# Kernel tuning notes

Measured on AMD Instinct MI355X. Metric: run time of the kernel, lower is better.

The kernel has to match this reference:

```python
import jax, jax.numpy as jnp
import numpy as np


def setup_inputs() -> dict:
    key = jax.random.key(0)
    k1, k2 = jax.random.split(key)
    x = jax.random.normal(k1, (32, 256, 32, 32), dtype=jnp.float32)
    emb = jax.random.uniform(k2, (256, 2048), dtype=jnp.float32)
    return {"x": x, "emb": emb}


def reference(x, emb):
    # x: (B, D, H, W), emb: (D, K)
    B, D = x.shape[0], x.shape[1]
    spatial = x.shape[2:]
    K = emb.shape[1]
    # flatten latents: (N, D) with N = B*H*W
    xf = jnp.moveaxis(x, 1, -1).reshape(-1, D)
    d2 = (jnp.sum(xf * xf, axis=-1, keepdims=True)
          - 2.0 * (xf @ emb)
          + jnp.sum(emb * emb, axis=0))  # (N, K)
    argmin = jnp.argmin(d2, axis=-1)  # (N,)
    q = jnp.take(emb.T, argmin, axis=0)  # (N, D) nearest codes
    out = q.reshape(B, *spatial, D)
    out = jnp.moveaxis(out, -1, 1)  # (B, D, H, W)
    return out
```

## Files before the change

### kernel.cpp

```cpp
#include <hip/hip_runtime.h>


typedef __attribute__((ext_vector_type(8))) _Float16 half8v;
typedef __attribute__((ext_vector_type(16))) float floatx16;
typedef unsigned int uint;
typedef unsigned short ushort;

#define DD 256
#define KK 2048
#define SS 1024
#define NN 32768
#define MT 128
#define NTT 256
#define CD 32
#define LDA 40
#define MFMA_F16 __builtin_amdgcn_mfma_f32_32x32x16_f16

union HU { _Float16 f; ushort u; };

__device__ __forceinline__ void split16(float v, ushort& h, ushort& l) {
    HU a, b;
    a.f = (_Float16)v;
    b.f = (_Float16)(v - (float)a.f);
    h = a.u; l = b.u;
}

__device__ __forceinline__ uint pk(ushort a, ushort b) {
    return (uint)a | ((uint)b << 16);
}

__global__ __launch_bounds__(256) void hn_kernel(const float* __restrict__ emb,
                                                 float* __restrict__ hn) {
    __shared__ float red[256];
    const int tid = threadIdx.x;
    const int k = blockIdx.x * 32 + (tid & 31);
    const int j = tid >> 5;
    float a = 0.f;
#pragma unroll
    for (int i = 0; i < 32; ++i) {
        float e = emb[(size_t)(j * 32 + i) * KK + k];
        a += e * e;
    }
    red[tid] = a;
    __syncthreads();
    if (j == 0) {
        float s = a;
#pragma unroll
        for (int g = 1; g < 8; ++g) s += red[g * 32 + (tid & 31)];
        hn[k] = 0.5f * s;
    }
}

__global__ __launch_bounds__(256) void pack_emb(const float* __restrict__ emb,
                                                uint4* __restrict__ epk) {
    int idx = blockIdx.x * 256 + threadIdx.x;
    int k = idx & (KK - 1);
    int q = idx >> 11;
    ushort h[8], l[8];
#pragma unroll
    for (int j = 0; j < 8; ++j) {
        float e = emb[(size_t)(8 * q + j) * KK + k];
        split16(e, h[j], l[j]);
    }
    uint4 H, L;
    H.x = pk(h[0], h[1]); H.y = pk(h[2], h[3]);
    H.z = pk(h[4], h[5]); H.w = pk(h[6], h[7]);
    L.x = pk(l[0], l[1]); L.y = pk(l[2], l[3]);
    L.z = pk(l[4], l[5]); L.w = pk(l[6], l[7]);
    epk[(size_t)(q * 2 + 0) * KK + k] = H;
    epk[(size_t)(q * 2 + 1) * KK + k] = L;
}

template <bool PRE>
__global__ __launch_bounds__(1024, 4) void vq_fused(
        const float* __restrict__ x, const float* __restrict__ emb,
        const float* __restrict__ hn, const uint4* __restrict__ epk,
        float* __restrict__ out) {
    __shared__ ushort Ah[2][MT * LDA], Al[2][MT * LDA];
    __shared__ ushort Bh[2][NTT * LDA], Bl[2][NTT * LDA];
    __shared__ float sv[4][MT];
    __shared__ int   sc[4][MT];
    __shared__ int   bc[MT];

    const int tid = threadIdx.x;
    const int lane = tid & 63;
    const int wid = tid >> 6;
    const int colk = lane & 31;
    const int half = lane >> 5;
    const int wm = (wid & 3) * 32;
    const int wn = (wid >> 2) * 64;

    const int base_n = blockIdx.x * MT;
    const int bq = base_n >> 10;
    const int sb = base_n & (SS - 1);

    const int lat_a = tid & 127;
    const int d2a = tid >> 7;
    const int cod_b = tid & 255;
    const int pB = (tid >> 8) & 1;
    const int oB = tid >> 9;

    const float* xA = x + ((size_t)bq * DD + 2 * d2a) * SS + sb + lat_a;

    floatx16 acc[2];
#pragma unroll
    for (int j = 0; j < 2; ++j) acc[j] = (floatx16)(0.0f);

    float bestv[16];
    int bestc[16];
#pragma unroll
    for (int r = 0; r < 16; ++r) { bestv[r] = 3.4e38f; bestc[r] = 0; }

    float fa0[4], fa1[4];
    uint4 u00, u01, u10, u11;
    float fb0[16], fb1[16];

    auto issueA = [&](int c, float (&fa)[4]) {
        const int dt = (c & 7) * CD;
        fa[0] = xA[(size_t)(dt + 0) * SS];
        fa[1] = xA[(size_t)(dt + 1) * SS];
        fa[2] = xA[(size_t)(dt + 16) * SS];
        fa[3] = xA[(size_t)(dt + 17) * SS];
    };
    auto issueB = [&](int c, uint4& a0, uint4& a1, float (&fb)[16]) {
        const int kt = c >> 3;
        const int dt = (c & 7) * CD;
        if constexpr (PRE) {
            const int qg = (dt >> 3) + 2 * oB;
            const size_t kb = (size_t)kt * NTT + cod_b;
            a0 = epk[(size_t)(qg * 2 + pB) * KK + kb];
            a1 = epk[(size_t)((qg + 1) * 2 + pB) * KK + kb];
        } else {
#pragma unroll
            for (int i = 0; i < 16; ++i)
                fb[i] = emb[(size_t)(dt + oB * 16 + i) * KK
                            + (size_t)kt * NTT + cod_b];
        }
    };
    auto stageWrite = [&](int nxt, float (&fa)[4], uint4& a0, uint4& a1,
                          float (&fb)[16]) {
        ushort h0, l0, h1, l1, h2, l2, h3, l3;
        split16(fa[0], h0, l0); split16(fa[1], h1, l1);
        split16(fa[2], h2, l2); split16(fa[3], h3, l3);
        *reinterpret_cast<uint*>(&Ah[nxt][lat_a * LDA + 2 * d2a]) = pk(h0, h1);
        *reinterpret_cast<uint*>(&Al[nxt][lat_a * LDA + 2 * d2a]) = pk(l0, l1);
        *reinterpret_cast<uint*>(&Ah[nxt][lat_a * LDA + 2 * d2a + 16]) = pk(h2, h3);
        *reinterpret_cast<uint*>(&Al[nxt][lat_a * LDA + 2 * d2a + 16]) = pk(l2, l3);
        uint4 w0, w1;
        if constexpr (PRE) {
            w0 = a0; w1 = a1;
        } else {
            ushort hh[16], ll[16];
#pragma unroll
            for (int i = 0; i < 16; ++i) split16(fb[i], hh[i], ll[i]);
            const ushort* s = pB ? ll : hh;
            w0.x = pk(s[0], s[1]);   w0.y = pk(s[2], s[3]);
            w0.z = pk(s[4], s[5]);   w0.w = pk(s[6], s[7]);
            w1.x = pk(s[8], s[9]);   w1.y = pk(s[10], s[11]);
            w1.z = pk(s[12], s[13]); w1.w = pk(s[14], s[15]);
        }
        ushort* Bp = pB ? &Bl[nxt][0] : &Bh[nxt][0];
        *reinterpret_cast<uint4*>(&Bp[cod_b * LDA + oB * 16]) = w0;
        *reinterpret_cast<uint4*>(&Bp[cod_b * LDA + oB * 16 + 8]) = w1;
    };
    auto compute = [&](int cur) {
        const int fo = colk * LDA + half * 8;
#pragma unroll
        for (int t = 0; t < 2; ++t) {
            const int o = t * 16;
            half8v ah = *reinterpret_cast<const half8v*>(&Ah[cur][fo + wm * LDA + o]);
            half8v al = *reinterpret_cast<const half8v*>(&Al[cur][fo + wm * LDA + o]);
            half8v bh0 = *reinterpret_cast<const half8v*>(&Bh[cur][fo + wn * LDA + o]);
            half8v bh1 = *reinterpret_cast<const half8v*>(&Bh[cur][fo + (wn + 32) * LDA + o]);
            half8v bl0 = *reinterpret_cast<const half8v*>(&Bl[cur][fo + wn * LDA + o]);
            half8v bl1 = *reinterpret_cast<const half8v*>(&Bl[cur][fo + (wn + 32) * LDA + o]);

            acc[0] = MFMA_F16(ah, bh0, acc[0], 0, 0, 0);
            acc[0] = MFMA_F16(ah, bl0, acc[0], 0, 0, 0);
            acc[0] = MFMA_F16(al, bh0, acc[0], 0, 0, 0);

            acc[1] = MFMA_F16(ah, bh1, acc[1], 0, 0, 0);
            acc[1] = MFMA_F16(ah, bl1, acc[1], 0, 0, 0);
            acc[1] = MFMA_F16(al, bh1, acc[1], 0, 0, 0);
        }
    };
    auto epilogue = [&](int kt) {
        const int cd0 = kt * NTT + wn + colk;
        const int cd1 = cd0 + 32;
        const float h0 = hn[cd0];
        const float h1 = hn[cd1];
#pragma unroll
        for (int r = 0; r < 16; ++r) {
            float s0 = h0 - acc[0][r];
            float s1 = h1 - acc[1][r];
            float v = s0; int cd = cd0;
            if (s1 < s0) { v = s1; cd = cd1; }
            if (v < bestv[r]) { bestv[r] = v; bestc[r] = cd; }
            acc[0][r] = 0.f;
            acc[1][r] = 0.f;
        }
    };

    issueA(0, fa0); issueB(0, u00, u01, fb0);
    stageWrite(0, fa0, u00, u01, fb0);
    issueA(1, fa1); issueB(1, u10, u11, fb1);
    __syncthreads();

    for (int cc = 0; cc < 32; ++cc) {
        const int c0 = cc * 2;
        if (c0 + 2 < 64) { issueA(c0 + 2, fa0); issueB(c0 + 2, u00, u01, fb0); }
        stageWrite(1, fa1, u10, u11, fb1);
        compute(0);
        __syncthreads();

        const int c1 = c0 + 1;
        if (c1 + 2 < 64) { issueA(c1 + 2, fa1); issueB(c1 + 2, u10, u11, fb1); }
        if (c1 + 1 < 64) { stageWrite(0, fa0, u00, u01, fb0); }
        compute(1);
        if ((c1 & 7) == 7) epilogue(c1 >> 3);
        __syncthreads();
    }

#pragma unroll
    for (int r = 0; r < 16; ++r) {
        float v = bestv[r];
        int cd = bestc[r];
#pragma unroll
        for (int mk = 1; mk < 32; mk <<= 1) {
            float ov = __shfl_xor(v, mk);
            int oc = __shfl_xor(cd, mk);
            if (ov < v || (ov == v && oc < cd)) { v = ov; cd = oc; }
        }
        if (colk == 0) {
            const int row = (r & 3) + 8 * (r >> 2) + 4 * half;
            sv[wid >> 2][wm + row] = v;
            sc[wid >> 2][wm + row] = cd;
        }
    }
    __syncthreads();
    if (tid < MT) {
        float v = sv[0][tid]; int cd = sc[0][tid];
#pragma unroll
        for (int g = 1; g < 4; ++g) {
            float ov = sv[g][tid]; int oc = sc[g][tid];
            if (ov < v || (ov == v && oc < cd)) { v = ov; cd = oc; }
        }
        bc[tid] = cd;
    }
    __syncthreads();
    {
        const int mq = tid & 31;
        const int dg = tid >> 5;
        const int k0 = bc[mq * 4 + 0];
        const int k1 = bc[mq * 4 + 1];
        const int k2 = bc[mq * 4 + 2];
        const int k3 = bc[mq * 4 + 3];
#pragma unroll 4
        for (int dd = 0; dd < 8; ++dd) {
            const int d = dg * 8 + dd;
            const float* er = emb + (size_t)d * KK;
            float4 o = make_float4(er[k0], er[k1], er[k2], er[k3]);
            reinterpret_cast<float4*>(&out[((size_t)bq * DD + d) * SS + sb])[mq] = o;
        }
    }
}

extern "C" void kernel_launch(void* const* d_in, const int* in_sizes, int n_in,
                              void* d_out, int out_size, void* d_ws, size_t ws_size,
                              hipStream_t stream) {
    const float* x = (const float*)d_in[0];
    const float* emb = (const float*)d_in[1];
    float* out = (float*)d_out;
    float* hn = (float*)d_ws;
    uint4* epk = (uint4*)((char*)d_ws + KK * sizeof(float));

    const size_t need = (size_t)KK * 4 + (size_t)32 * 2 * KK * 16;

    hipLaunchKernelGGL(hn_kernel, dim3(KK / 32), dim3(256), 0, stream, emb, hn);
    if (ws_size >= need) {
        hipLaunchKernelGGL(pack_emb, dim3(65536 / 256), dim3(256), 0, stream,
                           emb, epk);
        hipLaunchKernelGGL((vq_fused<true>), dim3(NN / MT), dim3(1024), 0, stream,
                           x, emb, hn, epk, out);
    } else {
        hipLaunchKernelGGL((vq_fused<false>), dim3(NN / MT), dim3(1024), 0, stream,
                           x, emb, hn, epk, out);
    }
}
```

Before: 211.5 us.

## Load A fragments directly from global into registers, dropping A shared-memory staging

Removes the double-buffered shared-memory tiles for the x operand. Each lane now loads its own MFMA A-fragment values straight from global memory and splits them into fp16 hi/lo parts in registers right before the MFMAs. This cuts LDS writes and reads and frees shared memory. In exchange, the A loads are issued in the same iteration they are used, no longer prefetched two stages ahead, so global latency is exposed. The 4 wn-waves also each reload the same x values redundantly.

```diff
diff --git a/kernel.cpp b/kernel.cpp
--- a/kernel.cpp
+++ b/kernel.cpp
@@ -17,6 +17,7 @@
 #define MFMA_F16 __builtin_amdgcn_mfma_f32_32x32x16_f16
 
 union HU { _Float16 f; ushort u; };
+union FragU { uint u[4]; half8v v; };
 
 __device__ __forceinline__ void split16(float v, ushort& h, ushort& l) {
     HU a, b;
@@ -76,7 +77,6 @@
         const float* __restrict__ x, const float* __restrict__ emb,
         const float* __restrict__ hn, const uint4* __restrict__ epk,
         float* __restrict__ out) {
-    __shared__ ushort Ah[2][MT * LDA], Al[2][MT * LDA];
     __shared__ ushort Bh[2][NTT * LDA], Bl[2][NTT * LDA];
     __shared__ float sv[4][MT];
     __shared__ int   sc[4][MT];
@@ -94,13 +94,11 @@
     const int bq = base_n >> 10;
     const int sb = base_n & (SS - 1);
 
-    const int lat_a = tid & 127;
-    const int d2a = tid >> 7;
     const int cod_b = tid & 255;
     const int pB = (tid >> 8) & 1;
     const int oB = tid >> 9;
 
-    const float* xA = x + ((size_t)bq * DD + 2 * d2a) * SS + sb + lat_a;
+    const float* xw = x + ((size_t)bq * DD + half * 8) * SS + sb + wm + colk;
 
     floatx16 acc[2];
 #pragma unroll
@@ -111,16 +109,17 @@
 #pragma unroll
     for (int r = 0; r < 16; ++r) { bestv[r] = 3.4e38f; bestc[r] = 0; }
 
-    float fa0[4], fa1[4];
     uint4 u00, u01, u10, u11;
     float fb0[16], fb1[16];
-
-    auto issueA = [&](int c, float (&fa)[4]) {
+    float fa[16];
+
+    auto issueA = [&](int c) {
         const int dt = (c & 7) * CD;
-        fa[0] = xA[(size_t)(dt + 0) * SS];
-        fa[1] = xA[(size_t)(dt + 1) * SS];
-        fa[2] = xA[(size_t)(dt + 16) * SS];
-        fa[3] = xA[(size_t)(dt + 17) * SS];
+#pragma unroll
+        for (int t = 0; t < 2; ++t)
+#pragma unroll
+            for (int j = 0; j < 8; ++j)
+                fa[t * 8 + j] = xw[(size_t)(dt + t * 16 + j) * SS];
     };
     auto issueB = [&](int c, uint4& a0, uint4& a1, float (&fb)[16]) {
         const int kt = c >> 3;
@@ -137,15 +136,7 @@
                             + (size_t)kt * NTT + cod_b];
         }
     };
-    auto stageWrite = [&](int nxt, float (&fa)[4], uint4& a0, uint4& a1,
-                          float (&fb)[16]) {
-        ushort h0, l0, h1, l1, h2, l2, h3, l3;
-        split16(fa[0], h0, l0); split16(fa[1], h1, l1);
-        split16(fa[2], h2, l2); split16(fa[3], h3, l3);
-        *reinterpret_cast<uint*>(&Ah[nxt][lat_a * LDA + 2 * d2a]) = pk(h0, h1);
-        *reinterpret_cast<uint*>(&Al[nxt][lat_a * LDA + 2 * d2a]) = pk(l0, l1);
-        *reinterpret_cast<uint*>(&Ah[nxt][lat_a * LDA + 2 * d2a + 16]) = pk(h2, h3);
-        *reinterpret_cast<uint*>(&Al[nxt][lat_a * LDA + 2 * d2a + 16]) = pk(l2, l3);
+    auto stageWrite = [&](int nxt, uint4& a0, uint4& a1, float (&fb)[16]) {
         uint4 w0, w1;
         if constexpr (PRE) {
             w0 = a0; w1 = a1;
@@ -167,21 +158,28 @@
         const int fo = colk * LDA + half * 8;
 #pragma unroll
         for (int t = 0; t < 2; ++t) {
+            ushort h[8], l[8];
+#pragma unroll
+            for (int j = 0; j < 8; ++j) split16(fa[t * 8 + j], h[j], l[j]);
+            FragU ah, al;
+#pragma unroll
+            for (int j = 0; j < 4; ++j) {
+                ah.u[j] = pk(h[2 * j], h[2 * j + 1]);
+                al.u[j] = pk(l[2 * j], l[2 * j + 1]);
+            }
             const int o = t * 16;
-            half8v ah = *reinterpret_cast<const half8v*>(&Ah[cur][fo + wm * LDA + o]);
-            half8v al = *reinterpret_cast<const half8v*>(&Al[cur][fo + wm * LDA + o]);
             half8v bh0 = *reinterpret_cast<const half8v*>(&Bh[cur][fo + wn * LDA + o]);
             half8v bh1 = *reinterpret_cast<const half8v*>(&Bh[cur][fo + (wn + 32) * LDA + o]);
             half8v bl0 = *reinterpret_cast<const half8v*>(&Bl[cur][fo + wn * LDA + o]);
             half8v bl1 = *reinterpret_cast<const half8v*>(&Bl[cur][fo + (wn + 32) * LDA + o]);
 
-            acc[0] = MFMA_F16(ah, bh0, acc[0], 0, 0, 0);
-            acc[0] = MFMA_F16(ah, bl0, acc[0], 0, 0, 0);
-            acc[0] = MFMA_F16(al, bh0, acc[0], 0, 0, 0);
-
-            acc[1] = MFMA_F16(ah, bh1, acc[1], 0, 0, 0);
-            acc[1] = MFMA_F16(ah, bl1, acc[1], 0, 0, 0);
-            acc[1] = MFMA_F16(al, bh1, acc[1], 0, 0, 0);
+            acc[0] = MFMA_F16(ah.v, bh0, acc[0], 0, 0, 0);
+            acc[0] = MFMA_F16(ah.v, bl0, acc[0], 0, 0, 0);
+            acc[0] = MFMA_F16(al.v, bh0, acc[0], 0, 0, 0);
+
+            acc[1] = MFMA_F16(ah.v, bh1, acc[1], 0, 0, 0);
+            acc[1] = MFMA_F16(ah.v, bl1, acc[1], 0, 0, 0);
+            acc[1] = MFMA_F16(al.v, bh1, acc[1], 0, 0, 0);
         }
     };
     auto epilogue = [&](int kt) {
@@ -201,21 +199,23 @@
         }
     };
 
-    issueA(0, fa0); issueB(0, u00, u01, fb0);
-    stageWrite(0, fa0, u00, u01, fb0);
-    issueA(1, fa1); issueB(1, u10, u11, fb1);
+    issueB(0, u00, u01, fb0);
+    stageWrite(0, u00, u01, fb0);
+    issueB(1, u10, u11, fb1);
     __syncthreads();
 
     for (int cc = 0; cc < 32; ++cc) {
         const int c0 = cc * 2;
-        if (c0 + 2 < 64) { issueA(c0 + 2, fa0); issueB(c0 + 2, u00, u01, fb0); }
-        stageWrite(1, fa1, u10, u11, fb1);
+        if (c0 + 2 < 64) { issueB(c0 + 2, u00, u01, fb0); }
+        issueA(c0);
+        stageWrite(1, u10, u11, fb1);
         compute(0);
         __syncthreads();
 
         const int c1 = c0 + 1;
-        if (c1 + 2 < 64) { issueA(c1 + 2, fa1); issueB(c1 + 2, u10, u11, fb1); }
-        if (c1 + 1 < 64) { stageWrite(0, fa0, u00, u01, fb0); }
+        if (c1 + 2 < 64) { issueB(c1 + 2, u10, u11, fb1); }
+        issueA(c1);
+        if (c1 + 1 < 64) { stageWrite(0, u00, u01, fb0); }
         compute(1);
         if ((c1 & 7) == 7) epilogue(c1 >> 3);
         __syncthreads();
```

Result: slower. 223.8 us (+5.8%).
